# Performance work log

Measured on AMD Instinct MI355X. Metric: run time of the kernel, lower is better.

Reference implementation:

```python
import jax, jax.numpy as jnp
import numpy as np

B, T, C = 2, 2048, 2048
NH, NKV = 16, 4
HD = C // NH  # 128


def _rope(x, cos, sin):
    d = x.shape[-1] // 2
    x1, x2 = x[..., :d], x[..., d:]
    return jnp.concatenate([x1 * cos + x2 * sin, -x1 * sin + x2 * cos], axis=-1)


def _rmsnorm(x):
    eps = jnp.finfo(x.dtype).eps
    return x * jax.lax.rsqrt(jnp.mean(jnp.square(x), axis=-1, keepdims=True) + eps)


def setup_inputs() -> dict:
    key = jax.random.key(0)
    ks = jax.random.split(key, 7)
    s = 0.02
    return {
        "x": jax.random.normal(ks[0], (B, T, C), jnp.float32),
        "cos": jax.random.normal(ks[1], (1, T, 1, HD // 2), jnp.float32),
        "sin": jax.random.normal(ks[2], (1, T, 1, HD // 2), jnp.float32),
        "wq": jax.random.normal(ks[3], (C, NH * HD), jnp.float32) * s,
        "wk": jax.random.normal(ks[4], (C, NKV * HD), jnp.float32) * s,
        "wv": jax.random.normal(ks[5], (C, NKV * HD), jnp.float32) * s,
        "wo": jax.random.normal(ks[6], (C, C), jnp.float32) * s,
    }


def reference(x, cos, sin, wq, wk, wv, wo):
    q = (x @ wq).reshape(B, T, NH, HD)
    k = (x @ wk).reshape(B, T, NKV, HD)
    v = (x @ wv).reshape(B, T, NKV, HD)
    q = _rmsnorm(_rope(q, cos, sin))
    k = _rmsnorm(_rope(k, cos, sin))
    # [B, H, T, D]
    q = q.transpose(0, 2, 1, 3)
    k = k.transpose(0, 2, 1, 3)
    v = v.transpose(0, 2, 1, 3)
    rep = NH // NKV
    k = jnp.repeat(k, rep, axis=1)
    v = jnp.repeat(v, rep, axis=1)
    scale = 1.0 / jnp.sqrt(jnp.float32(HD))
    scores = jnp.einsum("bhqd,bhkd->bhqk", q, k) * scale
    causal = jnp.tril(jnp.ones((T, T), bool))
    scores = jnp.where(causal, scores, jnp.finfo(scores.dtype).min)
    attn = jax.nn.softmax(scores, axis=-1)
    y = jnp.einsum("bhqk,bhkd->bhqd", attn, v)
    y = y.transpose(0, 2, 1, 3).reshape(B, T, C)
    return y @ wo
```

## Files before the change

kernel.cpp:

```cpp
#include <hip/hip_runtime.h>
#include <hip/hip_bf16.h>
#include <cstdint>

typedef unsigned short u16;
typedef __bf16 bf16x8 __attribute__((ext_vector_type(8)));
typedef float f32x4 __attribute__((ext_vector_type(4)));
typedef unsigned short u16x4 __attribute__((ext_vector_type(4)));
typedef unsigned uint2v __attribute__((ext_vector_type(2)));

#define B_ 2
#define T_ 2048
#define C_ 2048
#define NH_ 16
#define NKV_ 4
#define HD_ 128
#define K2_ 0.12752004650581538f

__device__ __forceinline__ u16 f2bf(float f) {
    unsigned u = __builtin_bit_cast(unsigned, f);
    unsigned r = u + 0x7FFFu + ((u >> 16) & 1u);
    return (u16)(r >> 16);
}

__device__ __forceinline__ float bf2f(u16 v) {
    unsigned u = ((unsigned)v) << 16;
    return __builtin_bit_cast(float, u);
}

__device__ __forceinline__ unsigned cvtpk(float a, float b) {
    unsigned r;
    asm("v_cvt_pk_bf16_f32 %0, %1, %2" : "=v"(r) : "v"(a), "v"(b));
    return r;
}

__device__ __forceinline__ void gl16(const void* g, void* l) {
    auto gp = reinterpret_cast<const __attribute__((address_space(1))) unsigned*>(
        reinterpret_cast<uintptr_t>(g));
    auto lp = reinterpret_cast<__attribute__((address_space(3))) unsigned*>(
        reinterpret_cast<uintptr_t>(l));
    __builtin_amdgcn_global_load_lds(gp, lp, 16, 0, 0);
}

__global__ void transpose_conv(const float* __restrict__ in, u16* __restrict__ out, int N) {
    __shared__ float tile[32][33];
    int n0 = blockIdx.x * 32, k0 = blockIdx.y * 32;
    int tx = threadIdx.x, ty = threadIdx.y;
#pragma unroll
    for (int i = 0; i < 4; ++i)
        tile[ty * 4 + i][tx] = in[(size_t)(k0 + ty * 4 + i) * N + n0 + tx];
    __syncthreads();
#pragma unroll
    for (int i = 0; i < 4; ++i)
        out[(size_t)(n0 + ty * 4 + i) * 2048 + k0 + tx] = f2bf(tile[tx][ty * 4 + i]);
}

__global__ void convert4(const float4* __restrict__ in, u16* __restrict__ out) {
    int i = blockIdx.x * 256 + threadIdx.x;
    float4 v = in[i];
    u16x4 o;
    o[0] = f2bf(v.x); o[1] = f2bf(v.y); o[2] = f2bf(v.z); o[3] = f2bf(v.w);
    ((u16x4*)out)[i] = o;
}

__global__ __launch_bounds__(256, 2) void gemm_bf16(const u16* __restrict__ A,
                                                    const u16* __restrict__ BT,
                                                    float* __restrict__ C, int N, int K) {
    __shared__ __align__(16) u16 As[2][128 * 64];
    __shared__ __align__(16) u16 Bs[2][128 * 64];
    int nwg = gridDim.x * gridDim.y;
    int bid = blockIdx.y * gridDim.x + blockIdx.x;
    int nb = (bid & 7) * (nwg >> 3) + (bid >> 3);
    int bx = nb % gridDim.x, by = nb / gridDim.x;

    int t = threadIdx.x;
    int w = t >> 6, l = t & 63;
    int wr = w >> 1, wc = w & 1;
    int lg = l >> 4, lr = l & 15;
    int m0 = by * 128, n0 = bx * 128;
    f32x4 acc[4][4] = {};

    size_t goff[4];
#pragma unroll
    for (int i = 0; i < 4; ++i) {
        int g = t + i * 256;
        goff[i] = (size_t)(g >> 3) * K * 2 + (size_t)(((g & 7) ^ ((g >> 3) & 7)) * 16);
    }
    const char* Ab = (const char*)A + (size_t)m0 * K * 2;
    const char* Bb = (const char*)BT + (size_t)n0 * K * 2;

    auto stage = [&](int kt, int buf) {
        char* Ad = (char*)As[buf] + t * 16;
        char* Bd = (char*)Bs[buf] + t * 16;
#pragma unroll
        for (int i = 0; i < 4; ++i) {
            gl16(Ab + (size_t)kt * 2 + goff[i], Ad + i * 4096);
            gl16(Bb + (size_t)kt * 2 + goff[i], Bd + i * 4096);
        }
    };

    stage(0, 0);
    int nk = K >> 6;
    for (int ki = 0; ki < nk; ++ki) {
        asm volatile("s_waitcnt vmcnt(0)" ::: "memory");
        __builtin_amdgcn_s_barrier();
        __builtin_amdgcn_sched_barrier(0);
        int cur = ki & 1;
        if (ki + 1 < nk) stage((ki + 1) * 64, cur ^ 1);
#pragma unroll
        for (int kk = 0; kk < 2; ++kk) {
            bf16x8 af[4], bfr[4];
#pragma unroll
            for (int m = 0; m < 4; ++m)
                af[m] = *(const bf16x8*)&As[cur][(wr * 64 + m * 16 + lr) * 64 +
                                                (((kk * 4 + lg) ^ (lr & 7)) * 8)];
#pragma unroll
            for (int n = 0; n < 4; ++n)
                bfr[n] = *(const bf16x8*)&Bs[cur][(wc * 64 + n * 16 + lr) * 64 +
                                                 (((kk * 4 + lg) ^ (lr & 7)) * 8)];
#pragma unroll
            for (int m = 0; m < 4; ++m)
#pragma unroll
                for (int n = 0; n < 4; ++n)
                    acc[m][n] = __builtin_amdgcn_mfma_f32_16x16x32_bf16(af[m], bfr[n], acc[m][n], 0, 0, 0);
        }
    }
#pragma unroll
    for (int m = 0; m < 4; ++m) {
        int row = m0 + wr * 64 + m * 16 + lg * 4;
#pragma unroll
        for (int n = 0; n < 4; ++n) {
            int col = n0 + wc * 64 + n * 16 + lr;
            float* Cp = C + (size_t)row * N + col;
#pragma unroll
            for (int r = 0; r < 4; ++r)
                Cp[(size_t)r * N] = acc[m][n][r];
        }
    }
}

__global__ __launch_bounds__(256, 2) void gemm_bf16o(const u16* __restrict__ A,
                                                     const u16* __restrict__ BT,
                                                     u16* __restrict__ C, int N, int K) {
    __shared__ __align__(16) u16 As[2][128 * 64];
    __shared__ __align__(16) u16 Bs[2][128 * 64];
    int nwg = gridDim.x * gridDim.y;
    int bid = blockIdx.y * gridDim.x + blockIdx.x;
    int nb = (bid & 7) * (nwg >> 3) + (bid >> 3);
    int bx = nb % gridDim.x, by = nb / gridDim.x;

    int t = threadIdx.x;
    int w = t >> 6, l = t & 63;
    int wr = w >> 1, wc = w & 1;
    int lg = l >> 4, lr = l & 15;
    int m0 = by * 128, n0 = bx * 128;
    f32x4 acc[4][4] = {};

    size_t goff[4];
#pragma unroll
    for (int i = 0; i < 4; ++i) {
        int g = t + i * 256;
        goff[i] = (size_t)(g >> 3) * K * 2 + (size_t)(((g & 7) ^ ((g >> 3) & 7)) * 16);
    }
    const char* Ab = (const char*)A + (size_t)m0 * K * 2;
    const char* Bb = (const char*)BT + (size_t)n0 * K * 2;

    auto stage = [&](int kt, int buf) {
        char* Ad = (char*)As[buf] + t * 16;
        char* Bd = (char*)Bs[buf] + t * 16;
#pragma unroll
        for (int i = 0; i < 4; ++i) {
            gl16(Ab + (size_t)kt * 2 + goff[i], Ad + i * 4096);
            gl16(Bb + (size_t)kt * 2 + goff[i], Bd + i * 4096);
        }
    };

    stage(0, 0);
    int nk = K >> 6;
    for (int ki = 0; ki < nk; ++ki) {
        asm volatile("s_waitcnt vmcnt(0)" ::: "memory");
        __builtin_amdgcn_s_barrier();
        __builtin_amdgcn_sched_barrier(0);
        int cur = ki & 1;
        if (ki + 1 < nk) stage((ki + 1) * 64, cur ^ 1);
#pragma unroll
        for (int kk = 0; kk < 2; ++kk) {
            bf16x8 af[4], bfr[4];
#pragma unroll
            for (int m = 0; m < 4; ++m)
                af[m] = *(const bf16x8*)&As[cur][(wr * 64 + m * 16 + lr) * 64 +
                                                (((kk * 4 + lg) ^ (lr & 7)) * 8)];
#pragma unroll
            for (int n = 0; n < 4; ++n)
                bfr[n] = *(const bf16x8*)&Bs[cur][(wc * 64 + n * 16 + lr) * 64 +
                                                 (((kk * 4 + lg) ^ (lr & 7)) * 8)];
#pragma unroll
            for (int m = 0; m < 4; ++m)
#pragma unroll
                for (int n = 0; n < 4; ++n)
                    acc[m][n] = __builtin_amdgcn_mfma_f32_16x16x32_bf16(af[m], bfr[n], acc[m][n], 0, 0, 0);
        }
    }
#pragma unroll
    for (int m = 0; m < 4; ++m) {
        int row = m0 + wr * 64 + m * 16 + lg * 4;
#pragma unroll
        for (int n = 0; n < 4; ++n) {
            int col = n0 + wc * 64 + n * 16 + lr;
            u16* Cp = C + (size_t)row * N + col;
#pragma unroll
            for (int r = 0; r < 4; ++r)
                Cp[(size_t)r * N] = f2bf(acc[m][n][r]);
        }
    }
}

__global__ void rope_rms(const u16* __restrict__ qkv, const float* __restrict__ cs,
                         const float* __restrict__ sn, u16* __restrict__ qh,
                         u16* __restrict__ kh) {
    int task = blockIdx.x * 4 + (threadIdx.x >> 6);
    int l = threadIdx.x & 63;
    const u16* in;
    u16* out;
    int tpos;
    float post = 1.0f;
    if (task < 65536) {
        int row = task >> 4, h = task & 15;
        in = qkv + (size_t)row * 3072 + h * 128;
        int b = row >> 11; tpos = row & 2047;
        out = qh + ((size_t)(b * NH_ + h) * T_ + tpos) * HD_;
        post = K2_;
    } else {
        int t2 = task - 65536;
        int row = t2 >> 2, h = t2 & 3;
        in = qkv + (size_t)row * 3072 + 2048 + h * 128;
        int b = row >> 11; tpos = row & 2047;
        out = kh + ((size_t)(b * NKV_ + h) * T_ + tpos) * HD_;
    }
    float x1 = bf2f(in[l]), x2 = bf2f(in[l + 64]);
    float c = cs[tpos * 64 + l], s = sn[tpos * 64 + l];
    float o1 = x1 * c + x2 * s;
    float o2 = -x1 * s + x2 * c;
    float ss = o1 * o1 + o2 * o2;
#pragma unroll
    for (int m = 1; m < 64; m <<= 1) ss += __shfl_xor(ss, m);
    float r = rsqrtf(ss * (1.0f / 128.0f) + 1.1920929e-07f) * post;
    out[l] = f2bf(o1 * r);
    out[l + 64] = f2bf(o2 * r);
}

__global__ void transpose_v(const u16* __restrict__ qkv, u16* __restrict__ vt) {
    __shared__ u16 tile[32][34];
    int t0 = blockIdx.x * 32;
    int d0 = blockIdx.y * 32;
    int bk = blockIdx.z;
    int b = bk >> 2, kvh = bk & 3;
    int tx = threadIdx.x, ty = threadIdx.y;
#pragma unroll
    for (int i = 0; i < 4; ++i)
        tile[ty * 4 + i][tx] =
            qkv[(size_t)(b * 2048 + t0 + ty * 4 + i) * 3072 + 2560 + kvh * 128 + d0 + tx];
    __syncthreads();
#pragma unroll
    for (int i = 0; i < 4; ++i)
        vt[((size_t)bk * 128 + d0 + ty * 4 + i) * 2048 + t0 + tx] = tile[tx][ty * 4 + i];
}

__global__ __launch_bounds__(256, 2) void attn(const u16* __restrict__ Q,
                                               const u16* __restrict__ Kk,
                                               const u16* __restrict__ V,
                                               u16* __restrict__ Y) {
    extern __shared__ __align__(16) u16 sm[];
    u16* Ks = sm;
    u16* Vs = sm + 16384;
    u16* Pb = sm + 24576;

    int bid = blockIdx.x;
    int xcd = bid & 7;
    int b = xcd >> 2, kvh = xcd & 3;
    int q = bid >> 3;
    int j = (q < 32) ? (63 - q) : (q - 32);
    int NN = (j >> 1) + 1;
    int t = threadIdx.x;
    int w = t >> 6, l = t & 63;
    int lg = l >> 4, lr = l & 15;
    int h = kvh * 4 + w;
    int qw = j * 32;

    const u16* Qp = Q + (size_t)(b * NH_ + h) * T_ * HD_;
    const u16* Kp = Kk + (size_t)(b * NKV_ + kvh) * T_ * HD_;
    const u16* Vp = V + (size_t)(b * NKV_ + kvh) * HD_ * T_;
    u16* Yp = Y + (size_t)(b * T_) * 2048 + h * HD_;
    u16* Pw = Pb + w * 512;

    size_t koff[4], voff[4];
#pragma unroll
    for (int i = 0; i < 4; ++i) {
        int g = t + i * 256;
        koff[i] = (size_t)(g >> 4) * 256 + (size_t)(((g & 15) ^ ((g >> 4) & 15)) * 16);
        voff[i] = (size_t)(g >> 3) * (T_ * 2) + (size_t)(((g & 7) ^ ((g >> 3) & 7)) * 16);
    }
    auto stageK = [&](int kv0, int buf) {
        const char* Kb = (const char*)Kp + (size_t)kv0 * 256;
        char* Kd = (char*)Ks + buf * 16384 + t * 16;
#pragma unroll
        for (int i = 0; i < 4; ++i) gl16(Kb + koff[i], Kd + i * 4096);
    };
    auto stageV = [&](int kv0) {
        const char* Vb = (const char*)Vp + (size_t)kv0 * 2;
        char* Vd = (char*)Vs + t * 16;
#pragma unroll
        for (int i = 0; i < 4; ++i) gl16(Vb + voff[i], Vd + i * 4096);
    };

    bf16x8 aq[2][4];
#pragma unroll
    for (int qf = 0; qf < 2; ++qf)
#pragma unroll
        for (int ch = 0; ch < 4; ++ch)
            aq[qf][ch] = *(const bf16x8*)(Qp + (size_t)(qw + qf * 16 + lr) * HD_ + ch * 32 + lg * 8);

    f32x4 acc[2][8] = {};
    float m2[2] = {-1e30f, -1e30f};
    float lp_[2] = {0.0f, 0.0f};

    stageK(0, 0);

    for (int gi = 0; gi < NN; ++gi) {
        asm volatile("s_waitcnt vmcnt(0)" ::: "memory");
        __builtin_amdgcn_s_barrier();
        __builtin_amdgcn_sched_barrier(0);
        int cur = gi & 1;
        int kv0 = gi * 64;
        stageV(kv0);
        __builtin_amdgcn_sched_barrier(0);
        int gn = (gi + 1 < NN) ? gi + 1 : 0;
        stageK(gn * 64, cur ^ 1);
        __builtin_amdgcn_sched_barrier(0);
        int kbase = cur * 8192;

        f32x4 sc[2][4] = {};
        __builtin_amdgcn_s_setprio(1);
#pragma unroll
        for (int ch = 0; ch < 4; ++ch)
#pragma unroll
            for (int kf = 0; kf < 4; ++kf) {
                bf16x8 bk = *(const bf16x8*)&Ks[kbase + (kf * 16 + lr) * 128 + (((ch * 4 + lg) ^ lr) * 8)];
                sc[0][kf] = __builtin_amdgcn_mfma_f32_16x16x32_bf16(bk, aq[0][ch], sc[0][kf], 0, 0, 0);
                sc[1][kf] = __builtin_amdgcn_mfma_f32_16x16x32_bf16(bk, aq[1][ch], sc[1][kf], 0, 0, 0);
            }
        __builtin_amdgcn_s_setprio(0);

        if (kv0 + 63 > qw) {
#pragma unroll
            for (int qf = 0; qf < 2; ++qf) {
                int qrow = qw + qf * 16 + lr;
#pragma unroll
                for (int kf = 0; kf < 4; ++kf)
#pragma unroll
                    for (int r = 0; r < 4; ++r) {
                        int key = kv0 + kf * 16 + 4 * lg + r;
                        if (key > qrow) sc[qf][kf][r] = -1e38f;
                    }
            }
        }
        float mx[2];
#pragma unroll
        for (int qf = 0; qf < 2; ++qf) {
            float m = sc[qf][0][0];
#pragma unroll
            for (int kf = 0; kf < 4; ++kf)
#pragma unroll
                for (int r = 0; r < 4; ++r) m = fmaxf(m, sc[qf][kf][r]);
            m = fmaxf(m, __shfl_xor(m, 16));
            m = fmaxf(m, __shfl_xor(m, 32));
            mx[qf] = m;
        }
        bool upd = (mx[0] > m2[0] + 8.0f) || (mx[1] > m2[1] + 8.0f);
        if (__any(upd)) {
#pragma unroll
            for (int qf = 0; qf < 2; ++qf) {
                float mn = fmaxf(m2[qf], mx[qf]);
                float rs = exp2f(m2[qf] - mn);
                m2[qf] = mn;
                lp_[qf] *= rs;
                float rs4[4];
#pragma unroll
                for (int r = 0; r < 4; ++r) rs4[r] = __shfl(rs, 4 * lg + r, 16);
#pragma unroll
                for (int oc = 0; oc < 8; ++oc)
#pragma unroll
                    for (int r = 0; r < 4; ++r) acc[qf][oc][r] *= rs4[r];
            }
        }
        bf16x8 ap[2][2];
#pragma unroll
        for (int kk = 0; kk < 2; ++kk) {
#pragma unroll
            for (int qf = 0; qf < 2; ++qf) {
                float ps = 0.0f;
#pragma unroll
                for (int kfl = 0; kfl < 2; ++kfl) {
                    int kf = kk * 2 + kfl;
                    float p0 = exp2f(sc[qf][kf][0] - m2[qf]);
                    float p1 = exp2f(sc[qf][kf][1] - m2[qf]);
                    float p2 = exp2f(sc[qf][kf][2] - m2[qf]);
                    float p3 = exp2f(sc[qf][kf][3] - m2[qf]);
                    ps += (p0 + p1) + (p2 + p3);
                    uint2v pk;
                    pk[0] = cvtpk(p0, p1);
                    pk[1] = cvtpk(p2, p3);
                    int g = 2 * kfl + (lg >> 1);
                    *(uint2v*)&Pw[lr * 32 + ((g ^ (lr & 3)) * 8) + (lg & 1) * 4] = pk;
                }
                lp_[qf] += ps;
                ap[qf][kk] = *(const bf16x8*)&Pw[lr * 32 + ((lg ^ (lr & 3)) * 8)];
            }
        }
        asm volatile("s_waitcnt vmcnt(4)" ::: "memory");
        __builtin_amdgcn_s_barrier();
        __builtin_amdgcn_sched_barrier(0);

        __builtin_amdgcn_s_setprio(1);
#pragma unroll
        for (int oc = 0; oc < 8; ++oc)
#pragma unroll
            for (int kk = 0; kk < 2; ++kk) {
                bf16x8 bv = *(const bf16x8*)&Vs[(oc * 16 + lr) * 64 +
                                                (((kk * 4 + lg) ^ (lr & 7)) * 8)];
                acc[0][oc] = __builtin_amdgcn_mfma_f32_16x16x32_bf16(ap[0][kk], bv, acc[0][oc], 0, 0, 0);
                acc[1][oc] = __builtin_amdgcn_mfma_f32_16x16x32_bf16(ap[1][kk], bv, acc[1][oc], 0, 0, 0);
            }
        __builtin_amdgcn_s_setprio(0);
    }
    asm volatile("s_waitcnt vmcnt(0)" ::: "memory");
#pragma unroll
    for (int qf = 0; qf < 2; ++qf) {
        float lt = lp_[qf];
        lt += __shfl_xor(lt, 16);
        lt += __shfl_xor(lt, 32);
        float inv = 1.0f / lt;
        float inv4[4];
#pragma unroll
        for (int r = 0; r < 4; ++r) inv4[r] = __shfl(inv, 4 * lg + r, 16);
#pragma unroll
        for (int oc = 0; oc < 8; ++oc)
#pragma unroll
            for (int r = 0; r < 4; ++r)
                Yp[(size_t)(qw + qf * 16 + 4 * lg + r) * 2048 + oc * 16 + lr] =
                    f2bf(acc[qf][oc][r] * inv4[r]);
    }
}

extern "C" void kernel_launch(void* const* d_in, const int* in_sizes, int n_in,
                              void* d_out, int out_size, void* d_ws, size_t ws_size,
                              hipStream_t stream) {
    const float* x    = (const float*)d_in[0];
    const float* cosT = (const float*)d_in[1];
    const float* sinT = (const float*)d_in[2];
    const float* wq   = (const float*)d_in[3];
    const float* wk   = (const float*)d_in[4];
    const float* wv   = (const float*)d_in[5];
    const float* wo   = (const float*)d_in[6];
    float* out = (float*)d_out;

    char* ws = (char*)d_ws;
    u16*   wqkvT = (u16*)(ws);
    u16*   woT   = (u16*)(ws + 12582912);
    u16*   xb    = (u16*)(ws + 20971520);
    u16*   qkv   = (u16*)(ws + 37748736);
    u16*   qh    = (u16*)(ws + 88080384);
    u16*   kh    = (u16*)(ws + 104857600);
    u16*   vt    = (u16*)(ws + 109051904);
    u16*   y     = xb;

    hipFuncSetAttribute(reinterpret_cast<const void*>(&attn),
                        hipFuncAttributeMaxDynamicSharedMemorySize, 53248);

    transpose_conv<<<dim3(64, 64), dim3(32, 8), 0, stream>>>(wq, wqkvT, 2048);
    transpose_conv<<<dim3(16, 64), dim3(32, 8), 0, stream>>>(wk, wqkvT + (size_t)2048 * 2048, 512);
    transpose_conv<<<dim3(16, 64), dim3(32, 8), 0, stream>>>(wv, wqkvT + (size_t)2560 * 2048, 512);
    transpose_conv<<<dim3(64, 64), dim3(32, 8), 0, stream>>>(wo, woT, 2048);
    convert4<<<8192, 256, 0, stream>>>((const float4*)x, xb);

    gemm_bf16o<<<dim3(24, 32), 256, 0, stream>>>(xb, wqkvT, qkv, 3072, 2048);

    rope_rms<<<20480, 256, 0, stream>>>(qkv, cosT, sinT, qh, kh);
    transpose_v<<<dim3(64, 4, 8), dim3(32, 8), 0, stream>>>(qkv, vt);

    attn<<<512, 256, 53248, stream>>>(qh, kh, vt, y);

    gemm_bf16<<<dim3(16, 32), 256, 0, stream>>>(y, woT, out, 2048, 2048);
}
```

Baseline: 202.0 us.

## Split long causal query tiles across two KV segments with a combine kernel

The attention kernel now splits the KV range of the 32 longest causal query tiles per head group into two halves, each handled by its own block. This raises the grid from 512 to 768 blocks and shortens the critical path. Each half writes unnormalized bf16 partial outputs plus row max and sum to workspace. A new combine kernel merges the halves with log-sum-exp rescaling. The cost is an extra launch, extra global traffic for the partials, and bf16 rounding of the unnormalized accumulators.

```diff
diff --git a/kernel.cpp b/kernel.cpp
--- a/kernel.cpp
+++ b/kernel.cpp
@@ -6,6 +6,7 @@
 typedef __bf16 bf16x8 __attribute__((ext_vector_type(8)));
 typedef float f32x4 __attribute__((ext_vector_type(4)));
 typedef unsigned short u16x4 __attribute__((ext_vector_type(4)));
+typedef unsigned short u16x8 __attribute__((ext_vector_type(8)));
 typedef unsigned uint2v __attribute__((ext_vector_type(2)));
 
 #define B_ 2
@@ -268,7 +269,9 @@
 __global__ __launch_bounds__(256, 2) void attn(const u16* __restrict__ Q,
                                                const u16* __restrict__ Kk,
                                                const u16* __restrict__ V,
-                                               u16* __restrict__ Y) {
+                                               u16* __restrict__ Y,
+                                               u16* __restrict__ Opart,
+                                               float2* __restrict__ Ml) {
     extern __shared__ __align__(16) u16 sm[];
     u16* Ks = sm;
     u16* Vs = sm + 16384;
@@ -277,9 +280,18 @@
     int bid = blockIdx.x;
     int xcd = bid & 7;
     int b = xcd >> 2, kvh = xcd & 3;
-    int q = bid >> 3;
-    int j = (q < 32) ? (63 - q) : (q - 32);
-    int NN = (j >> 1) + 1;
+    int tidx = bid >> 3;
+    int j, g0, g1, seg;
+    bool split;
+    if (tidx < 32) {
+        j = tidx; g0 = 0; g1 = (j >> 1) + 1; split = false; seg = 0;
+    } else if (tidx < 64) {
+        j = 95 - tidx; int NNs = (j >> 1) + 1;
+        g0 = 0; g1 = NNs >> 1; split = true; seg = 0;
+    } else {
+        j = 127 - tidx; int NNs = (j >> 1) + 1;
+        g0 = NNs >> 1; g1 = NNs; split = true; seg = 1;
+    }
     int t = threadIdx.x;
     int w = t >> 6, l = t & 63;
     int lg = l >> 4, lr = l & 15;
@@ -323,17 +335,17 @@
     float m2[2] = {-1e30f, -1e30f};
     float lp_[2] = {0.0f, 0.0f};
 
-    stageK(0, 0);
-
-    for (int gi = 0; gi < NN; ++gi) {
+    stageK(g0 * 64, 0);
+
+    for (int gi = g0; gi < g1; ++gi) {
         asm volatile("s_waitcnt vmcnt(0)" ::: "memory");
         __builtin_amdgcn_s_barrier();
         __builtin_amdgcn_sched_barrier(0);
-        int cur = gi & 1;
+        int cur = (gi - g0) & 1;
         int kv0 = gi * 64;
         stageV(kv0);
         __builtin_amdgcn_sched_barrier(0);
-        int gn = (gi + 1 < NN) ? gi + 1 : 0;
+        int gn = (gi + 1 < g1) ? gi + 1 : g0;
         stageK(gn * 64, cur ^ 1);
         __builtin_amdgcn_sched_barrier(0);
         int kbase = cur * 8192;
@@ -433,22 +445,80 @@
         __builtin_amdgcn_s_setprio(0);
     }
     asm volatile("s_waitcnt vmcnt(0)" ::: "memory");
+
+    float ltr[2];
 #pragma unroll
     for (int qf = 0; qf < 2; ++qf) {
         float lt = lp_[qf];
         lt += __shfl_xor(lt, 16);
         lt += __shfl_xor(lt, 32);
-        float inv = 1.0f / lt;
-        float inv4[4];
-#pragma unroll
-        for (int r = 0; r < 4; ++r) inv4[r] = __shfl(inv, 4 * lg + r, 16);
-#pragma unroll
-        for (int oc = 0; oc < 8; ++oc)
-#pragma unroll
-            for (int r = 0; r < 4; ++r)
-                Yp[(size_t)(qw + qf * 16 + 4 * lg + r) * 2048 + oc * 16 + lr] =
-                    f2bf(acc[qf][oc][r] * inv4[r]);
-    }
+        ltr[qf] = lt;
+    }
+
+    if (!split) {
+#pragma unroll
+        for (int qf = 0; qf < 2; ++qf) {
+            float inv = 1.0f / ltr[qf];
+            float inv4[4];
+#pragma unroll
+            for (int r = 0; r < 4; ++r) inv4[r] = __shfl(inv, 4 * lg + r, 16);
+#pragma unroll
+            for (int oc = 0; oc < 8; ++oc)
+#pragma unroll
+                for (int r = 0; r < 4; ++r)
+                    Yp[(size_t)(qw + qf * 16 + 4 * lg + r) * 2048 + oc * 16 + lr] =
+                        f2bf(acc[qf][oc][r] * inv4[r]);
+        }
+    } else {
+        int s32 = j - 32;
+        size_t pbase = (((size_t)(xcd * 32 + s32) * 2 + seg) * 4 + w);
+        u16* Op = Opart + pbase * 4096;
+        float2* mlp = Ml + pbase * 32;
+#pragma unroll
+        for (int qf = 0; qf < 2; ++qf)
+#pragma unroll
+            for (int oc = 0; oc < 8; ++oc)
+#pragma unroll
+                for (int r = 0; r < 4; ++r)
+                    Op[(qf * 16 + 4 * lg + r) * 128 + oc * 16 + lr] = f2bf(acc[qf][oc][r]);
+        if (lg == 0) {
+            mlp[lr] = float2{m2[0], ltr[0]};
+            mlp[16 + lr] = float2{m2[1], ltr[1]};
+        }
+    }
+}
+
+__global__ __launch_bounds__(256) void combine(const u16* __restrict__ Opart,
+                                               const float2* __restrict__ Ml,
+                                               u16* __restrict__ Y) {
+    int blk = blockIdx.x;
+    int w = blk & 3;
+    int s32 = (blk >> 2) & 31;
+    int xcd = blk >> 7;
+    int b = xcd >> 2, kvh = xcd & 3, h = kvh * 4 + w;
+    int qw = (32 + s32) * 32;
+    size_t p0 = (((size_t)(xcd * 32 + s32) * 2 + 0) * 4 + w);
+    size_t p1 = (((size_t)(xcd * 32 + s32) * 2 + 1) * 4 + w);
+    int t = threadIdx.x;
+    int row = t >> 3, c0 = (t & 7) * 16;
+    float2 a = Ml[p0 * 32 + row];
+    float2 c = Ml[p1 * 32 + row];
+    float M = fmaxf(a.x, c.x);
+    float w1 = exp2f(a.x - M), w2 = exp2f(c.x - M);
+    float inv = 1.0f / (w1 * a.y + w2 * c.y);
+    const u16* O1 = Opart + p0 * 4096 + row * 128 + c0;
+    const u16* O2 = Opart + p1 * 4096 + row * 128 + c0;
+    u16* Yp = Y + ((size_t)(b * T_) + qw + row) * 2048 + h * HD_ + c0;
+    u16x8 v1a = *(const u16x8*)O1, v1b = *(const u16x8*)(O1 + 8);
+    u16x8 v2a = *(const u16x8*)O2, v2b = *(const u16x8*)(O2 + 8);
+    u16x8 oa, ob;
+#pragma unroll
+    for (int i = 0; i < 8; ++i) {
+        oa[i] = f2bf((w1 * bf2f(v1a[i]) + w2 * bf2f(v2a[i])) * inv);
+        ob[i] = f2bf((w1 * bf2f(v1b[i]) + w2 * bf2f(v2b[i])) * inv);
+    }
+    *(u16x8*)Yp = oa;
+    *(u16x8*)(Yp + 8) = ob;
 }
 
 extern "C" void kernel_launch(void* const* d_in, const int* in_sizes, int n_in,
@@ -464,14 +534,16 @@
     float* out = (float*)d_out;
 
     char* ws = (char*)d_ws;
-    u16*   wqkvT = (u16*)(ws);
-    u16*   woT   = (u16*)(ws + 12582912);
-    u16*   xb    = (u16*)(ws + 20971520);
-    u16*   qkv   = (u16*)(ws + 37748736);
-    u16*   qh    = (u16*)(ws + 88080384);
-    u16*   kh    = (u16*)(ws + 104857600);
-    u16*   vt    = (u16*)(ws + 109051904);
-    u16*   y     = xb;
+    u16*    wqkvT = (u16*)(ws);
+    u16*    woT   = (u16*)(ws + 12582912);
+    u16*    xb    = (u16*)(ws + 20971520);
+    u16*    qkv   = (u16*)(ws + 37748736);
+    u16*    opart = (u16*)(ws + 62914560);
+    float2* mlbuf = (float2*)(ws + 79691776);
+    u16*    qh    = (u16*)(ws + 88080384);
+    u16*    kh    = (u16*)(ws + 104857600);
+    u16*    vt    = (u16*)(ws + 109051904);
+    u16*    y     = xb;
 
     hipFuncSetAttribute(reinterpret_cast<const void*>(&attn),
                         hipFuncAttributeMaxDynamicSharedMemorySize, 53248);
@@ -487,7 +559,8 @@
     rope_rms<<<20480, 256, 0, stream>>>(qkv, cosT, sinT, qh, kh);
     transpose_v<<<dim3(64, 4, 8), dim3(32, 8), 0, stream>>>(qkv, vt);
 
-    attn<<<512, 256, 53248, stream>>>(qh, kh, vt, y);
+    attn<<<768, 256, 53248, stream>>>(qh, kh, vt, y, opart, mlbuf);
+    combine<<<1024, 256, 0, stream>>>(opart, mlbuf, y);
 
     gemm_bf16<<<dim3(16, 32), 256, 0, stream>>>(y, woT, out, 2048, 2048);
 }
```

Result: no change. 201.9 us (-0.1%).
